# Performance work log

Hardware: AMD Instinct MI355X
Metric: run time of the kernel (lower is better)

Reference implementation:

```python
import jax, jax.numpy as jnp
import numpy as np

EPS = 1e-8  # torch.cosine_similarity default eps


def setup_inputs() -> dict:
    key = jax.random.key(0)
    ks = jax.random.split(key, 6)
    B, U, P, H = 256, 128, 64, 768
    utt_output = jax.random.normal(ks[0], (U, B, H), dtype=jnp.float32)
    pheno_output = jax.random.normal(ks[1], (P, B, H), dtype=jnp.float32)
    # Conv1d(in=U, out=U, kernel=P) weight: [out, in, kernel]
    w_utt = jax.random.normal(ks[2], (U, U, P), dtype=jnp.float32) / np.sqrt(U * P)
    b_utt = jax.random.normal(ks[3], (U,), dtype=jnp.float32) * 0.01
    # Conv1d(in=P, out=P, kernel=U) weight: [out, in, kernel]
    w_pheno = jax.random.normal(ks[4], (P, P, U), dtype=jnp.float32) / np.sqrt(P * U)
    b_pheno = jax.random.normal(ks[5], (P,), dtype=jnp.float32) * 0.01
    return {"utt_output": utt_output, "pheno_output": pheno_output,
            "w_utt": w_utt, "b_utt": b_utt, "w_pheno": w_pheno, "b_pheno": b_pheno}


def reference(utt_output, pheno_output, w_utt, b_utt, w_pheno, b_pheno):
    # [len, B, H] -> [B, len, H]
    u = jnp.swapaxes(utt_output, 0, 1)    # [B, U, H]
    p = jnp.swapaxes(pheno_output, 0, 1)  # [B, P, H]
    # cosine similarity matrix c[b,i,j] = <u_i, p_j> / (max(|u_i|,eps)*max(|p_j|,eps))
    un = u / jnp.maximum(jnp.linalg.norm(u, axis=-1, keepdims=True), EPS)
    pn = p / jnp.maximum(jnp.linalg.norm(p, axis=-1, keepdims=True), EPS)
    c = jnp.einsum('buh,bph->bup', un, pn)  # [B, U, P]
    # Conv1d with kernel covering the full width -> output length 1, i.e. an einsum
    row_logits = jnp.einsum('bup,oup->bo', c, w_utt) + b_utt        # [B, U]
    col_logits = jnp.einsum('bup,opu->bo', c, w_pheno) + b_pheno    # [B, P]
    row_attention = jax.nn.softmax(row_logits, axis=-1)
    col_attention = jax.nn.softmax(col_logits, axis=-1)
    return row_attention, col_attention
```

## Files before the change

### kernel.cpp

```cpp
#include <hip/hip_runtime.h>
#include <stdint.h>

#define Bn 256
#define Un 128
#define Pn 64
#define Hn 768
#define Ototal 192
#define KC 16

#define LDU 40
#define LDB 72

typedef short s4v __attribute__((ext_vector_type(4)));
typedef short s8v __attribute__((ext_vector_type(8)));
typedef float f4v __attribute__((ext_vector_type(4)));

__device__ __forceinline__ short f2bf(float x) {
  union { float f; uint32_t u; } c; c.f = x;
  uint32_t r = (c.u + 0x7fffu + ((c.u >> 16) & 1u)) >> 16;
  return (short)(r & 0xffffu);
}

__global__ void __launch_bounds__(256) convW(const float* __restrict__ w_utt,
                                             const float* __restrict__ w_ph,
                                             ushort* __restrict__ Wbf) {
  __shared__ float tile[64 * 129];
  const int bx = blockIdx.x;
  const int t = threadIdx.x;
  if (bx < 4096) {
    int idx = bx * 256 + t;
    Wbf[idx] = (ushort)f2bf(w_utt[idx]);
    return;
  }
  const int oc = bx - 4096;
  const float* src = w_ph + (size_t)oc * 8192;
#pragma unroll
  for (int itr = 0; itr < 8; ++itr) {
    int idx = itr * 1024 + t * 4;
    int j = idx >> 7, i = idx & 127;
    float4 v = *(const float4*)(src + idx);
    tile[j * 129 + i + 0] = v.x;
    tile[j * 129 + i + 1] = v.y;
    tile[j * 129 + i + 2] = v.z;
    tile[j * 129 + i + 3] = v.w;
  }
  __syncthreads();
  const size_t obase = (size_t)(128 + oc) * 8192;
#pragma unroll
  for (int itr = 0; itr < 8; ++itr) {
    int k = itr * 1024 + t * 4;
    int i = k >> 6, j = k & 63;
    s4v o4 = { f2bf(tile[(j + 0) * 129 + i]),
               f2bf(tile[(j + 1) * 129 + i]),
               f2bf(tile[(j + 2) * 129 + i]),
               f2bf(tile[(j + 3) * 129 + i]) };
    *(s4v*)&Wbf[obase + k] = o4;
  }
}

__global__ void __launch_bounds__(512) phaseA(const float* __restrict__ utt,
                                              const float* __restrict__ ph,
                                              ushort* __restrict__ Cbf) {
  const int bx = blockIdx.x;
  const int b = bx >> 1, half = bx & 1;
  const int t = threadIdx.x;
  const int w = t >> 6, l = t & 63;

  __shared__ short uA[64 * LDU];
  __shared__ short pB[64 * LDU];
  __shared__ float s_inu[64];
  __shared__ float s_inp[64];

  const int r  = t >> 3;
  const int cc = (t & 7) * 4;

  const size_t rstride = (size_t)Bn * Hn;
  const float* ubase = utt + (size_t)b * Hn + (size_t)(half * 64 + r) * rstride + cc;
  const float* pbase = ph  + (size_t)b * Hn + (size_t)r * rstride + cc;

  float4 ru = *(const float4*)ubase;
  float4 rp = *(const float4*)pbase;

  float ssu = 0.f, ssp = 0.f;
  f4v zero4 = {0.f, 0.f, 0.f, 0.f};
  f4v acc0 = zero4, acc1 = zero4;

  const int m  = l & 15;
  const int ko = (l >> 4) * 8;
  const int it = w & 3;
  const int jp = w >> 2;
  const int lw = r * LDU + (t & 7) * 4;

  const short* ab = &uA[(it * 16 + m) * LDU + ko];
  const short* bb = &pB[(jp * 32 + m) * LDU + ko];

  for (int c = 0; c < 24; ++c) {
    __syncthreads();
    float4 a = ru, p0 = rp;
    ssu += a.x*a.x + a.y*a.y + a.z*a.z + a.w*a.w;
    ssp += p0.x*p0.x + p0.y*p0.y + p0.z*p0.z + p0.w*p0.w;
    s4v au = { f2bf(a.x),  f2bf(a.y),  f2bf(a.z),  f2bf(a.w)  };
    s4v pp = { f2bf(p0.x), f2bf(p0.y), f2bf(p0.z), f2bf(p0.w) };
    *(s4v*)&uA[lw] = au;
    *(s4v*)&pB[lw] = pp;
    __syncthreads();
    if (c < 23) {
      ru = *(const float4*)(ubase + (c + 1) * 32);
      rp = *(const float4*)(pbase + (c + 1) * 32);
    }
    s8v af  = *(const s8v*)ab;
    s8v bf0 = *(const s8v*)bb;
    s8v bf1 = *(const s8v*)(bb + 16 * LDU);
    acc0 = __builtin_amdgcn_mfma_f32_16x16x32_bf16(af, bf0, acc0, 0, 0, 0);
    acc1 = __builtin_amdgcn_mfma_f32_16x16x32_bf16(af, bf1, acc1, 0, 0, 0);
  }

  ssu += __shfl_xor(ssu, 4); ssu += __shfl_xor(ssu, 2); ssu += __shfl_xor(ssu, 1);
  ssp += __shfl_xor(ssp, 4); ssp += __shfl_xor(ssp, 2); ssp += __shfl_xor(ssp, 1);
  if ((t & 7) == 0) {
    s_inu[r] = 1.f / fmaxf(sqrtf(ssu), 1e-8f);
    s_inp[r] = 1.f / fmaxf(sqrtf(ssp), 1e-8f);
  }
  __syncthreads();

  const int cl = l & 15;
  const int rq = (l >> 4) * 4;
#pragma unroll
  for (int jt = 0; jt < 2; ++jt) {
    int j = jp * 32 + jt * 16 + cl;
    float sj = s_inp[j];
    f4v a = (jt == 0) ? acc0 : acc1;
#pragma unroll
    for (int rr = 0; rr < 4; ++rr) {
      int il = it * 16 + rq + rr;
      float v = a[rr] * s_inu[il] * sj;
      Cbf[((size_t)b * Un + half * 64 + il) * Pn + j] = (ushort)f2bf(v);
    }
  }
}

__global__ void __launch_bounds__(256) phaseB(const ushort* __restrict__ Cbf,
                                              const ushort* __restrict__ Wbf,
                                              float* __restrict__ partial) {
  const int kc = blockIdx.x;
  const int mt = blockIdx.y;
  const int nt = blockIdx.z;
  const int t = threadIdx.x;
  const int w = t >> 6, l = t & 63;

  __shared__ short Ab[64 * LDB];
  __shared__ short Bb[64 * LDB];

  const int row = t >> 2;
  const int k16 = (t & 3) * 16;

  f4v zero4 = {0.f, 0.f, 0.f, 0.f};
  f4v acc[4] = {zero4, zero4, zero4, zero4};

  const ushort* Ag = Cbf + (size_t)(mt * 64 + row) * 8192 + kc * 512 + k16;
  const ushort* Bg = Wbf + (size_t)(nt * 64 + row) * 8192 + kc * 512 + k16;
  const int m  = l & 15;
  const int ko = (l >> 4) * 8;

  for (int c = 0; c < 8; ++c) {
    s8v av0 = *(const s8v*)(Ag + c * 64);
    s8v av1 = *(const s8v*)(Ag + c * 64 + 8);
    s8v bv0 = *(const s8v*)(Bg + c * 64);
    s8v bv1 = *(const s8v*)(Bg + c * 64 + 8);
    __syncthreads();
    *(s8v*)&Ab[row * LDB + k16]     = av0;
    *(s8v*)&Ab[row * LDB + k16 + 8] = av1;
    *(s8v*)&Bb[row * LDB + k16]     = bv0;
    *(s8v*)&Bb[row * LDB + k16 + 8] = bv1;
    __syncthreads();
#pragma unroll
    for (int ks = 0; ks < 2; ++ks) {
      s8v af = *(const s8v*)&Ab[(16 * w + m) * LDB + ks * 32 + ko];
#pragma unroll
      for (int jt = 0; jt < 4; ++jt) {
        s8v bf = *(const s8v*)&Bb[(16 * jt + m) * LDB + ks * 32 + ko];
        acc[jt] = __builtin_amdgcn_mfma_f32_16x16x32_bf16(af, bf, acc[jt], 0, 0, 0);
      }
    }
  }

  const int rq = (l >> 4) * 4;
#pragma unroll
  for (int jt = 0; jt < 4; ++jt) {
    int og = nt * 64 + 16 * jt + (l & 15);
#pragma unroll
    for (int r = 0; r < 4; ++r) {
      int bg = mt * 64 + 16 * w + rq + r;
      partial[((size_t)kc * Bn + bg) * Ototal + og] = acc[jt][r];
    }
  }
}

__global__ void __launch_bounds__(192) phaseC(const float* __restrict__ partial,
                                              const float* __restrict__ b_utt,
                                              const float* __restrict__ b_ph,
                                              float* __restrict__ out) {
  const int b = blockIdx.x;
  const int t = threadIdx.x;
  const int w = t >> 6, l = t & 63;

  float v = 0.f;
#pragma unroll
  for (int kc = 0; kc < KC; ++kc)
    v += partial[((size_t)kc * Bn + b) * Ototal + t];
  v += (t < Un) ? b_utt[t] : b_ph[t - Un];

  __shared__ float red[3];
  float mx = v;
  for (int o = 32; o >= 1; o >>= 1) mx = fmaxf(mx, __shfl_xor(mx, o));
  if (l == 0) red[w] = mx;
  __syncthreads();
  float gmax = (t < Un) ? fmaxf(red[0], red[1]) : red[2];
  float e = expf(v - gmax);
  float s = e;
  for (int o = 32; o >= 1; o >>= 1) s += __shfl_xor(s, o);
  __syncthreads();
  if (l == 0) red[w] = s;
  __syncthreads();
  float gs = (t < Un) ? (red[0] + red[1]) : red[2];
  float r = e / gs;
  if (t < Un) out[(size_t)b * Un + t] = r;
  else        out[(size_t)Bn * Un + (size_t)b * Pn + (t - Un)] = r;
}

extern "C" void kernel_launch(void* const* d_in, const int* in_sizes, int n_in,
                              void* d_out, int out_size, void* d_ws, size_t ws_size,
                              hipStream_t stream) {
  const float* utt   = (const float*)d_in[0];
  const float* ph    = (const float*)d_in[1];
  const float* w_utt = (const float*)d_in[2];
  const float* b_utt = (const float*)d_in[3];
  const float* w_ph  = (const float*)d_in[4];
  const float* b_ph  = (const float*)d_in[5];

  char* ws = (char*)d_ws;
  ushort* Cbf     = (ushort*)(ws);
  ushort* Wbf     = (ushort*)(ws + 4194304);
  float*  partial = (float*)(ws + 7340032);

  convW <<<dim3(4096 + 64), dim3(256), 0, stream>>>(w_utt, w_ph, Wbf);
  phaseA<<<dim3(2 * Bn), dim3(512), 0, stream>>>(utt, ph, Cbf);
  phaseB<<<dim3(KC, 4, 3), dim3(256), 0, stream>>>(Cbf, Wbf, partial);
  phaseC<<<dim3(Bn), dim3(192), 0, stream>>>(partial, b_utt, b_ph, (float*)d_out);
}
```

Before: 213.2 us.

## Widen phaseA K-chunks to 96 and double-buffer LDS to halve barriers

phaseA now stages 96 columns per iteration (three float4 per thread) instead of 32, running 8 iterations instead of 24. The LDS tiles are double-buffered, so each iteration needs one __syncthreads instead of two. Each thread issues more loads in flight and runs three MFMA k-steps per barrier. This cuts barrier and latency overhead in the memory-bound similarity phase, at the cost of more registers and more LDS.

Measured after the change: 213.2 us. About the same (-0.0%).

```diff
diff --git a/kernel.cpp b/kernel.cpp
--- a/kernel.cpp
+++ b/kernel.cpp
@@ -8,7 +8,9 @@
 #define Ototal 192
 #define KC 16
 
-#define LDU 40
+#define CH 96
+#define NIT 8
+#define LDU 104
 #define LDB 72
 
 typedef short s4v __attribute__((ext_vector_type(4)));
@@ -66,20 +68,24 @@
   const int t = threadIdx.x;
   const int w = t >> 6, l = t & 63;
 
-  __shared__ short uA[64 * LDU];
-  __shared__ short pB[64 * LDU];
+  __shared__ short uA[2][64 * LDU];
+  __shared__ short pB[2][64 * LDU];
   __shared__ float s_inu[64];
   __shared__ float s_inp[64];
 
   const int r  = t >> 3;
-  const int cc = (t & 7) * 4;
+  const int c12 = (t & 7) * 12;
 
   const size_t rstride = (size_t)Bn * Hn;
-  const float* ubase = utt + (size_t)b * Hn + (size_t)(half * 64 + r) * rstride + cc;
-  const float* pbase = ph  + (size_t)b * Hn + (size_t)r * rstride + cc;
-
-  float4 ru = *(const float4*)ubase;
-  float4 rp = *(const float4*)pbase;
+  const float* ubase = utt + (size_t)b * Hn + (size_t)(half * 64 + r) * rstride + c12;
+  const float* pbase = ph  + (size_t)b * Hn + (size_t)r * rstride + c12;
+
+  float4 u0 = *(const float4*)(ubase + 0);
+  float4 u1 = *(const float4*)(ubase + 4);
+  float4 u2 = *(const float4*)(ubase + 8);
+  float4 p0 = *(const float4*)(pbase + 0);
+  float4 p1 = *(const float4*)(pbase + 4);
+  float4 p2 = *(const float4*)(pbase + 8);
 
   float ssu = 0.f, ssp = 0.f;
   f4v zero4 = {0.f, 0.f, 0.f, 0.f};
@@ -89,30 +95,49 @@
   const int ko = (l >> 4) * 8;
   const int it = w & 3;
   const int jp = w >> 2;
-  const int lw = r * LDU + (t & 7) * 4;
-
-  const short* ab = &uA[(it * 16 + m) * LDU + ko];
-  const short* bb = &pB[(jp * 32 + m) * LDU + ko];
-
-  for (int c = 0; c < 24; ++c) {
+  const int lw = r * LDU + c12;
+
+#pragma unroll
+  for (int c = 0; c < NIT; ++c) {
+    const int s = c & 1;
+    float4 a0 = u0, a1 = u1, a2 = u2, q0 = p0, q1 = p1, q2 = p2;
+    ssu += a0.x*a0.x + a0.y*a0.y + a0.z*a0.z + a0.w*a0.w
+         + a1.x*a1.x + a1.y*a1.y + a1.z*a1.z + a1.w*a1.w
+         + a2.x*a2.x + a2.y*a2.y + a2.z*a2.z + a2.w*a2.w;
+    ssp += q0.x*q0.x + q0.y*q0.y + q0.z*q0.z + q0.w*q0.w
+         + q1.x*q1.x + q1.y*q1.y + q1.z*q1.z + q1.w*q1.w
+         + q2.x*q2.x + q2.y*q2.y + q2.z*q2.z + q2.w*q2.w;
+    s4v ua0 = { f2bf(a0.x), f2bf(a0.y), f2bf(a0.z), f2bf(a0.w) };
+    s4v ua1 = { f2bf(a1.x), f2bf(a1.y), f2bf(a1.z), f2bf(a1.w) };
+    s4v ua2 = { f2bf(a2.x), f2bf(a2.y), f2bf(a2.z), f2bf(a2.w) };
+    s4v pa0 = { f2bf(q0.x), f2bf(q0.y), f2bf(q0.z), f2bf(q0.w) };
+    s4v pa1 = { f2bf(q1.x), f2bf(q1.y), f2bf(q1.z), f2bf(q1.w) };
+    s4v pa2 = { f2bf(q2.x), f2bf(q2.y), f2bf(q2.z), f2bf(q2.w) };
+    *(s4v*)&uA[s][lw + 0] = ua0;
+    *(s4v*)&uA[s][lw + 4] = ua1;
+    *(s4v*)&uA[s][lw + 8] = ua2;
+    *(s4v*)&pB[s][lw + 0] = pa0;
+    *(s4v*)&pB[s][lw + 4] = pa1;
+    *(s4v*)&pB[s][lw + 8] = pa2;
     __syncthreads();
-    float4 a = ru, p0 = rp;
-    ssu += a.x*a.x + a.y*a.y + a.z*a.z + a.w*a.w;
-    ssp += p0.x*p0.x + p0.y*p0.y + p0.z*p0.z + p0.w*p0.w;
-    s4v au = { f2bf(a.x),  f2bf(a.y),  f2bf(a.z),  f2bf(a.w)  };
-    s4v pp = { f2bf(p0.x), f2bf(p0.y), f2bf(p0.z), f2bf(p0.w) };
-    *(s4v*)&uA[lw] = au;
-    *(s4v*)&pB[lw] = pp;
-    __syncthreads();
-    if (c < 23) {
-      ru = *(const float4*)(ubase + (c + 1) * 32);
-      rp = *(const float4*)(pbase + (c + 1) * 32);
-    }
-    s8v af  = *(const s8v*)ab;
-    s8v bf0 = *(const s8v*)bb;
-    s8v bf1 = *(const s8v*)(bb + 16 * LDU);
-    acc0 = __builtin_amdgcn_mfma_f32_16x16x32_bf16(af, bf0, acc0, 0, 0, 0);
-    acc1 = __builtin_amdgcn_mfma_f32_16x16x32_bf16(af, bf1, acc1, 0, 0, 0);
+    if (c + 1 < NIT) {
+      u0 = *(const float4*)(ubase + (c + 1) * CH + 0);
+      u1 = *(const float4*)(ubase + (c + 1) * CH + 4);
+      u2 = *(const float4*)(ubase + (c + 1) * CH + 8);
+      p0 = *(const float4*)(pbase + (c + 1) * CH + 0);
+      p1 = *(const float4*)(pbase + (c + 1) * CH + 4);
+      p2 = *(const float4*)(pbase + (c + 1) * CH + 8);
+    }
+    const short* ab = &uA[s][(it * 16 + m) * LDU + ko];
+    const short* bb = &pB[s][(jp * 32 + m) * LDU + ko];
+#pragma unroll
+    for (int ks = 0; ks < 3; ++ks) {
+      s8v af  = *(const s8v*)(ab + ks * 32);
+      s8v bf0 = *(const s8v*)(bb + ks * 32);
+      s8v bf1 = *(const s8v*)(bb + 16 * LDU + ks * 32);
+      acc0 = __builtin_amdgcn_mfma_f32_16x16x32_bf16(af, bf0, acc0, 0, 0, 0);
+      acc1 = __builtin_amdgcn_mfma_f32_16x16x32_bf16(af, bf1, acc1, 0, 0, 0);
+    }
   }
 
   ssu += __shfl_xor(ssu, 4); ssu += __shfl_xor(ssu, 2); ssu += __shfl_xor(ssu, 1);
```

## Split normalization and bf16 conversion into separate pass before cosine GEMM

Applied to the files above, without the earlier changes.

Adds a kernel that computes row norms, scales, converts to bf16, and writes inputs into a batch-major layout. The cosine GEMM then reads contiguous bf16 rows with large K chunks and fewer barriers, dropping the in-loop norm accumulation and post-scaling. This adds an extra write and read of the converted inputs plus a larger workspace requirement.

New measurement: 231.0 us. +8.4%, slower.

```diff
diff --git a/kernel.cpp b/kernel.cpp
--- a/kernel.cpp
+++ b/kernel.cpp
@@ -8,7 +8,7 @@
 #define Ototal 192
 #define KC 16
 
-#define LDU 40
+#define LDC 264
 #define LDB 72
 
 typedef short s4v __attribute__((ext_vector_type(4)));
@@ -19,6 +19,45 @@
   union { float f; uint32_t u; } c; c.f = x;
   uint32_t r = (c.u + 0x7fffu + ((c.u >> 16) & 1u)) >> 16;
   return (short)(r & 0xffffu);
+}
+
+__global__ void __launch_bounds__(256) normcvt(const float* __restrict__ utt,
+                                               const float* __restrict__ ph,
+                                               ushort* __restrict__ ubf,
+                                               ushort* __restrict__ pbf) {
+  const int wv = blockIdx.x * 4 + (threadIdx.x >> 6);
+  const int l = threadIdx.x & 63;
+
+  const float* src;
+  ushort* dst;
+  if (wv < Un * Bn) {
+    src = utt + (size_t)wv * Hn;
+    int i = wv >> 8, b = wv & 255;
+    dst = ubf + ((size_t)b * Un + i) * Hn;
+  } else {
+    int n2 = wv - Un * Bn;
+    src = ph + (size_t)n2 * Hn;
+    int j = n2 >> 8, b = n2 & 255;
+    dst = pbf + ((size_t)b * Pn + j) * Hn;
+  }
+
+  float4 v0 = *(const float4*)(src + l * 4);
+  float4 v1 = *(const float4*)(src + 256 + l * 4);
+  float4 v2 = *(const float4*)(src + 512 + l * 4);
+
+  float ss = v0.x*v0.x + v0.y*v0.y + v0.z*v0.z + v0.w*v0.w
+           + v1.x*v1.x + v1.y*v1.y + v1.z*v1.z + v1.w*v1.w
+           + v2.x*v2.x + v2.y*v2.y + v2.z*v2.z + v2.w*v2.w;
+  ss += __shfl_xor(ss, 32); ss += __shfl_xor(ss, 16); ss += __shfl_xor(ss, 8);
+  ss += __shfl_xor(ss, 4);  ss += __shfl_xor(ss, 2);  ss += __shfl_xor(ss, 1);
+  const float sc = 1.f / fmaxf(sqrtf(ss), 1e-8f);
+
+  s4v o0 = { f2bf(v0.x*sc), f2bf(v0.y*sc), f2bf(v0.z*sc), f2bf(v0.w*sc) };
+  s4v o1 = { f2bf(v1.x*sc), f2bf(v1.y*sc), f2bf(v1.z*sc), f2bf(v1.w*sc) };
+  s4v o2 = { f2bf(v2.x*sc), f2bf(v2.y*sc), f2bf(v2.z*sc), f2bf(v2.w*sc) };
+  *(s4v*)(dst + l * 4)       = o0;
+  *(s4v*)(dst + 256 + l * 4) = o1;
+  *(s4v*)(dst + 512 + l * 4) = o2;
 }
 
 __global__ void __launch_bounds__(256) convW(const float* __restrict__ w_utt,
@@ -58,30 +97,32 @@
   }
 }
 
-__global__ void __launch_bounds__(512) phaseA(const float* __restrict__ utt,
-                                              const float* __restrict__ ph,
-                                              ushort* __restrict__ Cbf) {
+__global__ void __launch_bounds__(512) gemmC(const ushort* __restrict__ ubf,
+                                             const ushort* __restrict__ pbf,
+                                             ushort* __restrict__ Cbf) {
   const int bx = blockIdx.x;
   const int b = bx >> 1, half = bx & 1;
   const int t = threadIdx.x;
   const int w = t >> 6, l = t & 63;
 
-  __shared__ short uA[64 * LDU];
-  __shared__ short pB[64 * LDU];
-  __shared__ float s_inu[64];
-  __shared__ float s_inp[64];
-
-  const int r  = t >> 3;
-  const int cc = (t & 7) * 4;
-
-  const size_t rstride = (size_t)Bn * Hn;
-  const float* ubase = utt + (size_t)b * Hn + (size_t)(half * 64 + r) * rstride + cc;
-  const float* pbase = ph  + (size_t)b * Hn + (size_t)r * rstride + cc;
-
-  float4 ru = *(const float4*)ubase;
-  float4 rp = *(const float4*)pbase;
-
-  float ssu = 0.f, ssp = 0.f;
+  __shared__ short As[64 * LDC];
+  __shared__ short Bs[64 * LDC];
+
+  const int row = t >> 3;
+  const int tc  = (t & 7) * 8;
+
+  const ushort* Au = ubf + ((size_t)b * Un + half * 64 + row) * Hn + tc;
+  const ushort* Pu = pbf + ((size_t)b * Pn + row) * Hn + tc;
+
+  s8v a0 = *(const s8v*)(Au + 0);
+  s8v a1 = *(const s8v*)(Au + 64);
+  s8v a2 = *(const s8v*)(Au + 128);
+  s8v a3 = *(const s8v*)(Au + 192);
+  s8v b0 = *(const s8v*)(Pu + 0);
+  s8v b1 = *(const s8v*)(Pu + 64);
+  s8v b2 = *(const s8v*)(Pu + 128);
+  s8v b3 = *(const s8v*)(Pu + 192);
+
   f4v zero4 = {0.f, 0.f, 0.f, 0.f};
   f4v acc0 = zero4, acc1 = zero4;
 
@@ -89,52 +130,53 @@
   const int ko = (l >> 4) * 8;
   const int it = w & 3;
   const int jp = w >> 2;
-  const int lw = r * LDU + (t & 7) * 4;
-
-  const short* ab = &uA[(it * 16 + m) * LDU + ko];
-  const short* bb = &pB[(jp * 32 + m) * LDU + ko];
-
-  for (int c = 0; c < 24; ++c) {
-    __syncthreads();
-    float4 a = ru, p0 = rp;
-    ssu += a.x*a.x + a.y*a.y + a.z*a.z + a.w*a.w;
-    ssp += p0.x*p0.x + p0.y*p0.y + p0.z*p0.z + p0.w*p0.w;
-    s4v au = { f2bf(a.x),  f2bf(a.y),  f2bf(a.z),  f2bf(a.w)  };
-    s4v pp = { f2bf(p0.x), f2bf(p0.y), f2bf(p0.z), f2bf(p0.w) };
-    *(s4v*)&uA[lw] = au;
-    *(s4v*)&pB[lw] = pp;
-    __syncthreads();
-    if (c < 23) {
-      ru = *(const float4*)(ubase + (c + 1) * 32);
-      rp = *(const float4*)(pbase + (c + 1) * 32);
-    }
-    s8v af  = *(const s8v*)ab;
-    s8v bf0 = *(const s8v*)bb;
-    s8v bf1 = *(const s8v*)(bb + 16 * LDU);
-    acc0 = __builtin_amdgcn_mfma_f32_16x16x32_bf16(af, bf0, acc0, 0, 0, 0);
-    acc1 = __builtin_amdgcn_mfma_f32_16x16x32_bf16(af, bf1, acc1, 0, 0, 0);
-  }
-
-  ssu += __shfl_xor(ssu, 4); ssu += __shfl_xor(ssu, 2); ssu += __shfl_xor(ssu, 1);
-  ssp += __shfl_xor(ssp, 4); ssp += __shfl_xor(ssp, 2); ssp += __shfl_xor(ssp, 1);
-  if ((t & 7) == 0) {
-    s_inu[r] = 1.f / fmaxf(sqrtf(ssu), 1e-8f);
-    s_inp[r] = 1.f / fmaxf(sqrtf(ssp), 1e-8f);
-  }
-  __syncthreads();
+  const int lw = row * LDC + tc;
+
+  const short* ab = &As[(it * 16 + m) * LDC + ko];
+  const short* bb = &Bs[(jp * 32 + m) * LDC + ko];
+
+#pragma unroll
+  for (int s = 0; s < 3; ++s) {
+    __syncthreads();
+    *(s8v*)&As[lw + 0]   = a0;
+    *(s8v*)&As[lw + 64]  = a1;
+    *(s8v*)&As[lw + 128] = a2;
+    *(s8v*)&As[lw + 192] = a3;
+    *(s8v*)&Bs[lw + 0]   = b0;
+    *(s8v*)&Bs[lw + 64]  = b1;
+    *(s8v*)&Bs[lw + 128] = b2;
+    *(s8v*)&Bs[lw + 192] = b3;
+    __syncthreads();
+    if (s + 1 < 3) {
+      a0 = *(const s8v*)(Au + (s + 1) * 256 + 0);
+      a1 = *(const s8v*)(Au + (s + 1) * 256 + 64);
+      a2 = *(const s8v*)(Au + (s + 1) * 256 + 128);
+      a3 = *(const s8v*)(Au + (s + 1) * 256 + 192);
+      b0 = *(const s8v*)(Pu + (s + 1) * 256 + 0);
+      b1 = *(const s8v*)(Pu + (s + 1) * 256 + 64);
+      b2 = *(const s8v*)(Pu + (s + 1) * 256 + 128);
+      b3 = *(const s8v*)(Pu + (s + 1) * 256 + 192);
+    }
+#pragma unroll
+    for (int ks = 0; ks < 8; ++ks) {
+      s8v af  = *(const s8v*)(ab + ks * 32);
+      s8v bf0 = *(const s8v*)(bb + ks * 32);
+      s8v bf1 = *(const s8v*)(bb + 16 * LDC + ks * 32);
+      acc0 = __builtin_amdgcn_mfma_f32_16x16x32_bf16(af, bf0, acc0, 0, 0, 0);
+      acc1 = __builtin_amdgcn_mfma_f32_16x16x32_bf16(af, bf1, acc1, 0, 0, 0);
+    }
+  }
 
   const int cl = l & 15;
   const int rq = (l >> 4) * 4;
 #pragma unroll
   for (int jt = 0; jt < 2; ++jt) {
     int j = jp * 32 + jt * 16 + cl;
-    float sj = s_inp[j];
     f4v a = (jt == 0) ? acc0 : acc1;
 #pragma unroll
     for (int rr = 0; rr < 4; ++rr) {
       int il = it * 16 + rq + rr;
-      float v = a[rr] * s_inu[il] * sj;
-      Cbf[((size_t)b * Un + half * 64 + il) * Pn + j] = (ushort)f2bf(v);
+      Cbf[((size_t)b * Un + half * 64 + il) * Pn + j] = (ushort)f2bf(a[rr]);
     }
   }
 }
@@ -242,9 +284,12 @@
   ushort* Cbf     = (ushort*)(ws);
   ushort* Wbf     = (ushort*)(ws + 4194304);
   float*  partial = (float*)(ws + 7340032);
-
-  convW <<<dim3(4096 + 64), dim3(256), 0, stream>>>(w_utt, w_ph, Wbf);
-  phaseA<<<dim3(2 * Bn), dim3(512), 0, stream>>>(utt, ph, Cbf);
-  phaseB<<<dim3(KC, 4, 3), dim3(256), 0, stream>>>(Cbf, Wbf, partial);
-  phaseC<<<dim3(Bn), dim3(192), 0, stream>>>(partial, b_utt, b_ph, (float*)d_out);
-}
+  ushort* ubf     = (ushort*)(ws + 10485760);
+  ushort* pbf     = (ushort*)(ws + 10485760 + 50331648);
+
+  normcvt<<<dim3(12288), dim3(256), 0, stream>>>(utt, ph, ubf, pbf);
+  convW  <<<dim3(4096 + 64), dim3(256), 0, stream>>>(w_utt, w_ph, Wbf);
+  gemmC  <<<dim3(2 * Bn), dim3(512), 0, stream>>>(ubf, pbf, Cbf);
+  phaseB <<<dim3(KC, 4, 3), dim3(256), 0, stream>>>(Cbf, Wbf, partial);
+  phaseC <<<dim3(Bn), dim3(192), 0, stream>>>(partial, b_utt, b_ph, (float*)d_out);
+}
```
